# Performance work log

Measured on AMD Instinct MI355X. Metric: run time of the kernel, lower is better.

Reference implementation:

```python
import jax, jax.numpy as jnp
import numpy as np
from math import sqrt

B, D, N, L, H, P = 32, 64, 254, 16, 128, 96  # batch, channels, patch_num, patch_len, hidden, pred_len


def positional_encoding(n, d):
    # standard sinusoidal PE, shape (n, d)
    pos = np.arange(n)[:, None].astype(np.float32)
    div = np.exp(np.arange(0, d, 2).astype(np.float32) * (-np.log(10000.0) / d))
    pe = np.zeros((n, d), dtype=np.float32)
    pe[:, 0::2] = np.sin(pos * div)
    pe[:, 1::2] = np.cos(pos * div)
    return jnp.asarray(pe)


def setup_inputs() -> dict:
    key = jax.random.key(0)
    ks = jax.random.split(key, 7)
    s = 0.05
    return {
        "x": jax.random.normal(ks[0], (B, D, N, L), dtype=jnp.float32),
        "W_enc": jax.random.normal(ks[1], (L, H), dtype=jnp.float32) * s,
        "b_enc": jax.random.normal(ks[2], (H,), dtype=jnp.float32) * s,
        "W1": jax.random.normal(ks[3], (L, H), dtype=jnp.float32) * s,
        "b1": jax.random.normal(ks[4], (H,), dtype=jnp.float32) * s,
        "W2": jax.random.normal(ks[5], (H, P), dtype=jnp.float32) * s,
        "b2": jax.random.normal(ks[6], (P,), dtype=jnp.float32) * s,
        "pos_embed": positional_encoding(N, H),  # buffer, not learned
    }


def reference(x, W_enc, b_enc, W1, b1, W2, b2, pos_embed):
    p = x  # detached clone in torch; same values
    # encode patches: (B,D,N,L) @ (L,H) -> (B,D,N,H), plus PE (N,H) broadcast
    c = jnp.einsum("bdnl,lh->bdnh", x, W_enc) + b_enc + pos_embed
    # score_i = sum_j c_i . c_j / sqrt(H)  ==  c_i . (sum_j c_j) / sqrt(H)
    csum = jnp.sum(c, axis=-2, keepdims=True)            # (B,D,1,H)
    score = jnp.sum(c * csum, axis=-1, keepdims=True) / sqrt(H)  # (B,D,N,1)
    weight = score / jnp.sum(jnp.abs(score), axis=-2, keepdims=True)
    pooled = jnp.sum(x * weight, axis=-2)                # (B,D,L)
    # FeedForward (dropout inactive at eval)
    h = jax.nn.leaky_relu(pooled @ W1 + b1, negative_slope=0.2)
    out = h @ W2 + b2                                    # (B,D,P)
    return out.transpose(0, 2, 1), p                     # (B,P,D), (B,D,N,L)
```

## Files before the change

kernel.cpp:

```cpp
#include <hip/hip_runtime.h>

#define B_ 32
#define D_ 64
#define N_ 254
#define L_ 16
#define H_ 128
#define P_ 96
#define PAIRS (B_*D_)
#define XPAIR (N_*L_)
#define OUT0  (B_*P_*D_)

#define WS_M    128
#define WS_VK   384
#define WS_BW   400
#define WS_BK   416
#define WS_G    432
#define WS_PK   4496
#define WS_KP   4752

typedef float f32x4 __attribute__((ext_vector_type(4)));

__global__ __launch_bounds__(256) void preK(const float* __restrict__ pos,
                                            float* __restrict__ ws) {
    __shared__ float red[256];
    int t = threadIdx.x;
    int h = t & 127, j = t >> 7;
    int n0 = blockIdx.x * 16;
    float acc = 0.f;
    #pragma unroll
    for (int r = 0; r < 8; r++) {
        int n = n0 + j + 2 * r;
        if (n < N_) acc += pos[n * H_ + h];
    }
    red[t] = acc;
    __syncthreads();
    if (t < 128) ws[WS_KP + blockIdx.x * 128 + t] = red[t] + red[t + 128];
}

__global__ __launch_bounds__(128) void pre2b(const float* __restrict__ W_enc,
                                             const float* __restrict__ b_enc,
                                             const float* __restrict__ pos,
                                             float* __restrict__ ws) {
    __shared__ float Ks[128], bL[128], pLDS[128], red[128], red2[128];
    __shared__ float WL[2048];
    int t = threadIdx.x;
    int n = blockIdx.x;

    {
        float b = b_enc[t];
        float s = 254.f * b;
        #pragma unroll
        for (int g = 0; g < 16; g++) s += ws[WS_KP + g * 128 + t];
        Ks[t] = s;
        bL[t] = b;
    }

    if (n < N_) {
        pLDS[t] = pos[n * H_ + t];
        __syncthreads();
        {
            int l = t >> 3, c = t & 7;
            const float* w = W_enc + l * H_ + c * 16;
            const float* p = pLDS + c * 16;
            float s = 0.f;
            #pragma unroll
            for (int i = 0; i < 16; i++) s += p[i] * w[i];
            red[t] = s;
            red2[t] = pLDS[t] * Ks[t];
        }
        __syncthreads();
        if (t < 16) {
            float s = 0.f;
            #pragma unroll
            for (int c = 0; c < 8; c++) s += red[t * 8 + c];
            ws[WS_G + n * 16 + t] = s;
        }
        if (t >= 64) {
            int lane = t - 64;
            float s = red2[lane] + red2[lane + 64];
            for (int off = 32; off; off >>= 1) s += __shfl_down(s, off);
            if (lane == 0) ws[WS_PK + n] = s;
        }
    } else {
        for (int i = t; i < 512; i += 128) {
            float4 v = ((const float4*)W_enc)[i];
            float* p = &WL[i * 4];
            p[0] = v.x; p[1] = v.y; p[2] = v.z; p[3] = v.w;
        }
        __syncthreads();
        #pragma unroll
        for (int e0 = 0; e0 < 2; e0++) {
            int e = e0 * 128 + t;
            int l1 = e >> 4, l2 = e & 15;
            float s = 0.f;
            for (int h = 0; h < H_; h++) s += WL[l1 * H_ + h] * WL[l2 * H_ + h];
            ws[WS_M + e] = s;
        }
        if (t < 16) {
            float s1 = 0.f, s2 = 0.f;
            for (int h = 0; h < H_; h++) {
                float w = WL[t * H_ + h];
                s1 += w * Ks[h];
                s2 += w * bL[h];
            }
            ws[WS_VK + t] = s1;
            ws[WS_BW + t] = s2;
        }
        if (t == 16) {
            float s = 0.f;
            for (int h = 0; h < H_; h++) s += bL[h] * Ks[h];
            ws[WS_BK] = s;
        }
    }
}

__global__ __launch_bounds__(256) void mainker(const float* __restrict__ x,
                                               const float* __restrict__ W1,
                                               const float* __restrict__ b1,
                                               const float* __restrict__ W2,
                                               const float* __restrict__ b2,
                                               const float* __restrict__ ws,
                                               float* __restrict__ out) {
    __shared__ f32x4 red4[256];
    __shared__ float scoreS[256];
    __shared__ float xsS[16], vS[16], pooledS[16], hS[128];
    __shared__ float s0S, denomS;

    int t  = threadIdx.x;
    int bd = blockIdx.x;
    int q  = t & 3, r0 = t >> 2;

    const f32x4* xv = (const f32x4*)(x + (size_t)bd * XPAIR);
    f32x4*       cv = (f32x4*)(out + OUT0) + (size_t)bd * (XPAIR / 4);

    f32x4 v0 = xv[t];
    f32x4 v1 = xv[t + 256];
    f32x4 v2 = xv[t + 512];
    f32x4 v3 = {0.f, 0.f, 0.f, 0.f};
    bool has3 = (t < 248);
    if (has3) v3 = xv[t + 768];

    cv[t]       = v0;
    cv[t + 256] = v1;
    cv[t + 512] = v2;
    if (has3) cv[t + 768] = v3;

    red4[t] = v0 + v1 + v2 + v3;
    __syncthreads();
    if (t < 64) red4[t] = red4[t] + red4[t + 64] + red4[t + 128] + red4[t + 192];
    __syncthreads();

    if (t < 16) {
        float xsv = 0.f;
        #pragma unroll
        for (int m = 0; m < 16; m++) xsv += red4[m * 4 + (t >> 2)][t & 3];
        xsS[t] = xsv;
        float s = ws[WS_VK + t];
        #pragma unroll
        for (int l2 = 0; l2 < 16; l2++) s += __shfl(xsv, l2) * ws[WS_M + l2 * 16 + t];
        vS[t] = s;
        float s0p = xsv * ws[WS_BW + t];
        #pragma unroll
        for (int off = 8; off; off >>= 1) s0p += __shfl_down(s0p, off);
        if (t == 0) s0S = ws[WS_BK] + s0p;
    }
    __syncthreads();

    {
        float vq0 = vS[4*q], vq1 = vS[4*q+1], vq2 = vS[4*q+2], vq3 = vS[4*q+3];
        float xq0 = xsS[4*q], xq1 = xsS[4*q+1], xq2 = xsS[4*q+2], xq3 = xsS[4*q+3];
        #pragma unroll
        for (int k = 0; k < 4; k++) {
            if (k < 3 || has3) {
                int rk = r0 + 64 * k;
                f32x4 xk = (k == 0) ? v0 : (k == 1) ? v1 : (k == 2) ? v2 : v3;
                f32x4 g  = *(const f32x4*)(ws + WS_G + rk * 16 + 4 * q);
                float s = xk[0]*vq0 + xk[1]*vq1 + xk[2]*vq2 + xk[3]*vq3
                        + xq0*g[0] + xq1*g[1] + xq2*g[2] + xq3*g[3];
                s += __shfl_xor(s, 1);
                s += __shfl_xor(s, 2);
                if (q == 0) scoreS[rk] = s + s0S + ws[WS_PK + rk];
            }
        }
    }
    __syncthreads();

    if (t < 64) {
        float s = 0.f;
        for (int n = t; n < N_; n += 64) s += fabsf(scoreS[n]);
        for (int off = 32; off; off >>= 1) s += __shfl_down(s, off);
        if (t == 0) denomS = s;
    }
    {
        f32x4 p4 = v0 * scoreS[r0] + v1 * scoreS[r0 + 64] + v2 * scoreS[r0 + 128];
        if (has3) p4 += v3 * scoreS[r0 + 192];
        red4[t] = p4;
    }
    __syncthreads();
    if (t < 64) red4[t] = red4[t] + red4[t + 64] + red4[t + 128] + red4[t + 192];
    __syncthreads();
    if (t < 16) {
        float invd = 1.0f / denomS;
        float s = 0.f;
        #pragma unroll
        for (int m = 0; m < 16; m++) s += red4[m * 4 + (t >> 2)][t & 3];
        pooledS[t] = s * invd;
    }
    __syncthreads();

    if (t < 128) {
        float s = b1[t];
        #pragma unroll
        for (int l = 0; l < 16; l++) s += pooledS[l] * W1[l * H_ + t];
        hS[t] = s > 0.f ? s : 0.2f * s;
    }
    __syncthreads();

    if (t < 96) {
        float s = b2[t];
        for (int j = 0; j < 128; j++) s += hS[j] * W2[j * P_ + t];
        int b = bd >> 6, d = bd & 63;
        out[b * (P_ * D_) + t * D_ + d] = s;
    }
}

extern "C" void kernel_launch(void* const* d_in, const int* in_sizes, int n_in,
                              void* d_out, int out_size, void* d_ws, size_t ws_size,
                              hipStream_t stream) {
    const float* x     = (const float*)d_in[0];
    const float* W_enc = (const float*)d_in[1];
    const float* b_enc = (const float*)d_in[2];
    const float* W1    = (const float*)d_in[3];
    const float* b1    = (const float*)d_in[4];
    const float* W2    = (const float*)d_in[5];
    const float* b2    = (const float*)d_in[6];
    const float* pos   = (const float*)d_in[7];
    float* ws  = (float*)d_ws;
    float* out = (float*)d_out;

    hipLaunchKernelGGL(preK,   dim3(16),    dim3(256), 0, stream, pos, ws);
    hipLaunchKernelGGL(pre2b,  dim3(255),   dim3(128), 0, stream, W_enc, b_enc, pos, ws);
    hipLaunchKernelGGL(mainker, dim3(PAIRS), dim3(256), 0, stream, x, W1, b1, W2, b2, ws, out);
}
```

Measured before the change: 119.4 us.

## Process one (b,d) pair per wavefront with shuffle reductions instead of block barriers

The main kernel now assigns each (batch, channel) pair to a single 64-lane wavefront, four pairs per block, instead of a whole 256-thread block per pair. Each lane holds 16 float4 rows in registers. All reductions (column sums, score denominators, pooled sums) use cross-lane shuffles rather than shared memory and __syncthreads. The feed-forward layers are spread across all 64 lanes instead of a 16/128/96-thread subset. The aim is to remove barrier and LDS round-trip latency and idle threads. In exchange, per-thread register pressure rises and each wave does more serial loads, which may lower occupancy.

New measurement: 135.0 us. 13.0% more time.

```diff
diff --git a/kernel.cpp b/kernel.cpp
--- a/kernel.cpp
+++ b/kernel.cpp
@@ -20,6 +20,16 @@
 
 typedef float f32x4 __attribute__((ext_vector_type(4)));
 
+__device__ __forceinline__ f32x4 sx4(f32x4 v, int m) {
+    f32x4 r;
+    r[0] = __shfl_xor(v[0], m); r[1] = __shfl_xor(v[1], m);
+    r[2] = __shfl_xor(v[2], m); r[3] = __shfl_xor(v[3], m);
+    return r;
+}
+__device__ __forceinline__ float dot4(f32x4 a, f32x4 b) {
+    return a[0]*b[0] + a[1]*b[1] + a[2]*b[2] + a[3]*b[3];
+}
+
 __global__ __launch_bounds__(256) void preK(const float* __restrict__ pos,
                                             float* __restrict__ ws) {
     __shared__ float red[256];
@@ -121,107 +131,103 @@
                                                const float* __restrict__ b2,
                                                const float* __restrict__ ws,
                                                float* __restrict__ out) {
-    __shared__ f32x4 red4[256];
-    __shared__ float scoreS[256];
-    __shared__ float xsS[16], vS[16], pooledS[16], hS[128];
-    __shared__ float s0S, denomS;
-
-    int t  = threadIdx.x;
-    int bd = blockIdx.x;
-    int q  = t & 3, r0 = t >> 2;
+    __shared__ float hS[4 * 128];
+
+    int tid = threadIdx.x;
+    int w = tid >> 6, i = tid & 63;
+    int q = i & 3, k = i >> 2;
+    int bd = blockIdx.x * 4 + w;
 
     const f32x4* xv = (const f32x4*)(x + (size_t)bd * XPAIR);
     f32x4*       cv = (f32x4*)(out + OUT0) + (size_t)bd * (XPAIR / 4);
-
-    f32x4 v0 = xv[t];
-    f32x4 v1 = xv[t + 256];
-    f32x4 v2 = xv[t + 512];
-    f32x4 v3 = {0.f, 0.f, 0.f, 0.f};
-    bool has3 = (t < 248);
-    if (has3) v3 = xv[t + 768];
-
-    cv[t]       = v0;
-    cv[t + 256] = v1;
-    cv[t + 512] = v2;
-    if (has3) cv[t + 768] = v3;
-
-    red4[t] = v0 + v1 + v2 + v3;
-    __syncthreads();
-    if (t < 64) red4[t] = red4[t] + red4[t + 64] + red4[t + 128] + red4[t + 192];
-    __syncthreads();
-
-    if (t < 16) {
-        float xsv = 0.f;
-        #pragma unroll
-        for (int m = 0; m < 16; m++) xsv += red4[m * 4 + (t >> 2)][t & 3];
-        xsS[t] = xsv;
-        float s = ws[WS_VK + t];
-        #pragma unroll
-        for (int l2 = 0; l2 < 16; l2++) s += __shfl(xsv, l2) * ws[WS_M + l2 * 16 + t];
-        vS[t] = s;
-        float s0p = xsv * ws[WS_BW + t];
-        #pragma unroll
-        for (int off = 8; off; off >>= 1) s0p += __shfl_down(s0p, off);
-        if (t == 0) s0S = ws[WS_BK] + s0p;
-    }
-    __syncthreads();
-
-    {
-        float vq0 = vS[4*q], vq1 = vS[4*q+1], vq2 = vS[4*q+2], vq3 = vS[4*q+3];
-        float xq0 = xsS[4*q], xq1 = xsS[4*q+1], xq2 = xsS[4*q+2], xq3 = xsS[4*q+3];
-        #pragma unroll
-        for (int k = 0; k < 4; k++) {
-            if (k < 3 || has3) {
-                int rk = r0 + 64 * k;
-                f32x4 xk = (k == 0) ? v0 : (k == 1) ? v1 : (k == 2) ? v2 : v3;
-                f32x4 g  = *(const f32x4*)(ws + WS_G + rk * 16 + 4 * q);
-                float s = xk[0]*vq0 + xk[1]*vq1 + xk[2]*vq2 + xk[3]*vq3
-                        + xq0*g[0] + xq1*g[1] + xq2*g[2] + xq3*g[3];
-                s += __shfl_xor(s, 1);
-                s += __shfl_xor(s, 2);
-                if (q == 0) scoreS[rk] = s + s0S + ws[WS_PK + rk];
-            }
-        }
-    }
-    __syncthreads();
-
-    if (t < 64) {
-        float s = 0.f;
-        for (int n = t; n < N_; n += 64) s += fabsf(scoreS[n]);
-        for (int off = 32; off; off >>= 1) s += __shfl_down(s, off);
-        if (t == 0) denomS = s;
-    }
-    {
-        f32x4 p4 = v0 * scoreS[r0] + v1 * scoreS[r0 + 64] + v2 * scoreS[r0 + 128];
-        if (has3) p4 += v3 * scoreS[r0 + 192];
-        red4[t] = p4;
-    }
-    __syncthreads();
-    if (t < 64) red4[t] = red4[t] + red4[t + 64] + red4[t + 128] + red4[t + 192];
-    __syncthreads();
-    if (t < 16) {
-        float invd = 1.0f / denomS;
-        float s = 0.f;
-        #pragma unroll
-        for (int m = 0; m < 16; m++) s += red4[m * 4 + (t >> 2)][t & 3];
-        pooledS[t] = s * invd;
-    }
-    __syncthreads();
-
-    if (t < 128) {
-        float s = b1[t];
-        #pragma unroll
-        for (int l = 0; l < 16; l++) s += pooledS[l] * W1[l * H_ + t];
-        hS[t] = s > 0.f ? s : 0.2f * s;
-    }
-    __syncthreads();
-
-    if (t < 96) {
-        float s = b2[t];
-        for (int j = 0; j < 128; j++) s += hS[j] * W2[j * P_ + t];
-        int b = bd >> 6, d = bd & 63;
-        out[b * (P_ * D_) + t * D_ + d] = s;
-    }
+    bool full = (i < 56);
+
+    f32x4 xq[16];
+    #pragma unroll
+    for (int r = 0; r < 15; r++) xq[r] = xv[r * 64 + i];
+    xq[15] = full ? xv[15 * 64 + i] : (f32x4){0.f, 0.f, 0.f, 0.f};
+    #pragma unroll
+    for (int r = 0; r < 15; r++) cv[r * 64 + i] = xq[r];
+    if (full) cv[15 * 64 + i] = xq[15];
+
+    f32x4 a = xq[0];
+    #pragma unroll
+    for (int r = 1; r < 16; r++) a = a + xq[r];
+    a = a + sx4(a, 4); a = a + sx4(a, 8); a = a + sx4(a, 16); a = a + sx4(a, 32);
+    f32x4 xsb = sx4(a, 1);
+    f32x4 xsc = sx4(a, 2);
+    f32x4 xsd = sx4(xsb, 2);
+
+    f32x4 vq = *(const f32x4*)(ws + WS_VK + 4 * q);
+    float s0 = ws[WS_BK];
+    int u0 = q, u1 = q ^ 1, u2 = q ^ 2, u3 = q ^ 3;
+    #pragma unroll
+    for (int c = 0; c < 4; c++) {
+        vq = vq + a[c]   * *(const f32x4*)(ws + WS_M + (4 * u0 + c) * 16 + 4 * q);
+        vq = vq + xsb[c] * *(const f32x4*)(ws + WS_M + (4 * u1 + c) * 16 + 4 * q);
+        vq = vq + xsc[c] * *(const f32x4*)(ws + WS_M + (4 * u2 + c) * 16 + 4 * q);
+        vq = vq + xsd[c] * *(const f32x4*)(ws + WS_M + (4 * u3 + c) * 16 + 4 * q);
+        s0 += a[c] * ws[WS_BW + 4 * u0 + c] + xsb[c] * ws[WS_BW + 4 * u1 + c]
+            + xsc[c] * ws[WS_BW + 4 * u2 + c] + xsd[c] * ws[WS_BW + 4 * u3 + c];
+    }
+
+    float scores[16];
+    #pragma unroll
+    for (int r = 0; r < 16; r++) {
+        int n = 16 * r + k;
+        f32x4 g = *(const f32x4*)(ws + WS_G + n * 16 + 4 * q);
+        float s = dot4(xq[r], vq) + dot4(a, g);
+        s += __shfl_xor(s, 1);
+        s += __shfl_xor(s, 2);
+        s += s0 + ws[WS_PK + n];
+        if (n >= N_) s = 0.f;
+        scores[r] = s;
+    }
+
+    float dn = 0.f;
+    #pragma unroll
+    for (int r = 0; r < 16; r++) dn += fabsf(scores[r]);
+    dn += __shfl_xor(dn, 1);  dn += __shfl_xor(dn, 2);  dn += __shfl_xor(dn, 4);
+    dn += __shfl_xor(dn, 8);  dn += __shfl_xor(dn, 16); dn += __shfl_xor(dn, 32);
+    float inv = 4.0f / dn;
+
+    f32x4 pp = xq[0] * scores[0];
+    #pragma unroll
+    for (int r = 1; r < 16; r++) pp = pp + xq[r] * scores[r];
+    pp = pp + sx4(pp, 4); pp = pp + sx4(pp, 8); pp = pp + sx4(pp, 16); pp = pp + sx4(pp, 32);
+    pp = pp * inv;
+    f32x4 pb = sx4(pp, 1);
+    f32x4 pc = sx4(pp, 2);
+    f32x4 pd = sx4(pb, 2);
+
+    float h0 = b1[i], h1 = b1[64 + i];
+    #pragma unroll
+    for (int c = 0; c < 4; c++) {
+        h0 += pp[c] * W1[(4 * u0 + c) * H_ + i]      + pb[c] * W1[(4 * u1 + c) * H_ + i]
+            + pc[c] * W1[(4 * u2 + c) * H_ + i]      + pd[c] * W1[(4 * u3 + c) * H_ + i];
+        h1 += pp[c] * W1[(4 * u0 + c) * H_ + 64 + i] + pb[c] * W1[(4 * u1 + c) * H_ + 64 + i]
+            + pc[c] * W1[(4 * u2 + c) * H_ + 64 + i] + pd[c] * W1[(4 * u3 + c) * H_ + 64 + i];
+    }
+    h0 = h0 > 0.f ? h0 : 0.2f * h0;
+    h1 = h1 > 0.f ? h1 : 0.2f * h1;
+    hS[w * 128 + i] = h0;
+    hS[w * 128 + 64 + i] = h1;
+
+    const f32x4* h4 = (const f32x4*)(hS + w * 128);
+    float s1 = b2[i];
+    float s2 = (i < 32) ? b2[64 + i] : 0.f;
+    #pragma unroll
+    for (int j4 = 0; j4 < 32; j4++) {
+        f32x4 hv = h4[j4];
+        s1 += hv[0] * W2[(4 * j4 + 0) * P_ + i] + hv[1] * W2[(4 * j4 + 1) * P_ + i]
+            + hv[2] * W2[(4 * j4 + 2) * P_ + i] + hv[3] * W2[(4 * j4 + 3) * P_ + i];
+        if (i < 32)
+            s2 += hv[0] * W2[(4 * j4 + 0) * P_ + 64 + i] + hv[1] * W2[(4 * j4 + 1) * P_ + 64 + i]
+                + hv[2] * W2[(4 * j4 + 2) * P_ + 64 + i] + hv[3] * W2[(4 * j4 + 3) * P_ + 64 + i];
+    }
+    int b = bd >> 6, d = bd & 63;
+    out[b * (P_ * D_) + i * D_ + d] = s1;
+    if (i < 32) out[b * (P_ * D_) + (64 + i) * D_ + d] = s2;
 }
 
 extern "C" void kernel_launch(void* const* d_in, const int* in_sizes, int n_in,
@@ -238,7 +244,7 @@
     float* ws  = (float*)d_ws;
     float* out = (float*)d_out;
 
-    hipLaunchKernelGGL(preK,   dim3(16),    dim3(256), 0, stream, pos, ws);
-    hipLaunchKernelGGL(pre2b,  dim3(255),   dim3(128), 0, stream, W_enc, b_enc, pos, ws);
-    hipLaunchKernelGGL(mainker, dim3(PAIRS), dim3(256), 0, stream, x, W1, b1, W2, b2, ws, out);
-}
+    hipLaunchKernelGGL(preK,   dim3(16),        dim3(256), 0, stream, pos, ws);
+    hipLaunchKernelGGL(pre2b,  dim3(255),       dim3(128), 0, stream, W_enc, b_enc, pos, ws);
+    hipLaunchKernelGGL(mainker, dim3(PAIRS / 4), dim3(256), 0, stream, x, W1, b1, W2, b2, ws, out);
+}
```
